# Kernel optimization log

Hardware: AMD Instinct MI355X
Metric: run time of the kernel (lower is better)

## Reference

```python
import jax, jax.numpy as jnp
import numpy as np

B, N, E = 16, 512, 6144          # graphs, sites/graph, edges/graph
D = 256                          # embed_dimension
RBF_DIM = 128
M = 6                            # num_messages
MAXZ = 84                        # max_atomic_num
INIT_MAX_DIST, INIT_GAP = 7.0, 30.0


def setup_inputs() -> dict:
    key = jax.random.key(0)
    ks = jax.random.split(key, 20)
    s = 0.02
    inp = {
        "site_class": jax.random.randint(ks[0], (B, N), 0, MAXZ, dtype=jnp.int64),
        "distance": jax.random.uniform(ks[1], (B, E), dtype=jnp.float32) * INIT_MAX_DIST,
        "connectivity": jax.random.randint(ks[2], (B, E, 2), 0, N, dtype=jnp.int64),
        # learned parameters
        "atom_emb": jax.random.normal(ks[3], (MAXZ, D), jnp.float32) * s,
        "mean_emb": jnp.zeros((MAXZ, 1), jnp.float32),  # Constant(output_bias=0.0)
        "centers": jnp.arange(RBF_DIM, dtype=jnp.float32) * (INIT_MAX_DIST / RBF_DIM),
        "gap": jnp.float32(INIT_GAP),
        "bond_W": jax.random.normal(ks[4], (RBF_DIM, D), jnp.float32) * s,
        "bond_b": jnp.zeros((D,), jnp.float32),
        "offset_W": jax.random.normal(ks[5], (D, 1), jnp.float32) * 1e-6,
        "offset_b": jnp.zeros((1,), jnp.float32),
        # per-message EdgeUpdate ConcatDense: Dense(2D, relu) -> Dense(D), input 3D
        "edge_W1": jax.random.normal(ks[6], (M, 3 * D, 2 * D), jnp.float32) * s,
        "edge_b1": jnp.zeros((M, 2 * D), jnp.float32),
        "edge_W2": jax.random.normal(ks[7], (M, 2 * D, D), jnp.float32) * s,
        "edge_b2": jnp.zeros((M, D), jnp.float32),
        # per-message NodeUpdate ConcatDense: input 2D
        "node_W1": jax.random.normal(ks[8], (M, 2 * D, 2 * D), jnp.float32) * s,
        "node_b1": jnp.zeros((M, 2 * D), jnp.float32),
        "node_W2": jax.random.normal(ks[9], (M, 2 * D, D), jnp.float32) * s,
        "node_b2": jnp.zeros((M, D), jnp.float32),
    }
    return inp


def _gather(x, idx):
    # x: [B, N, D], idx: [B, E] -> [B, E, D]
    return x[jnp.arange(x.shape[0])[:, None], idx]


def reference(site_class, distance, connectivity,
              atom_emb, mean_emb, centers, gap, bond_W, bond_b,
              offset_W, offset_b,
              edge_W1, edge_b1, edge_W2, edge_b2,
              node_W1, node_b1, node_W2, node_b2):
    atom_mask = site_class != 0                     # [B, N] (Embedding mask_zero)
    bond_mask = distance != 0.0                     # [B, E] (RBFExpansion mask)

    atom_state = atom_emb[site_class]               # [B, N, D]
    atom_mean = mean_emb[site_class]                # [B, N, 1]

    # RBF expansion: exp(-gap * (d - centers)^2), masked distances -> 1.0
    d = distance[..., None]
    d = jnp.where(d != 0.0, d, 1.0)
    rbf = jnp.exp(-((d - centers) ** 2) * gap)      # [B, E, RBF_DIM]
    bond_state = rbf @ bond_W + bond_b              # [B, E, D]

    bidx = jnp.arange(site_class.shape[0])[:, None]
    idx0 = connectivity[..., 0]                     # scatter target
    idx1 = connectivity[..., 1]                     # message source

    n_msg = edge_W1.shape[0]
    for i in range(n_msg):
        # EdgeUpdate: concat(bond, src_atom, tgt_atom) -> Dense(2D, relu) -> Dense(D)
        src = _gather(atom_state, idx1)
        tgt = _gather(atom_state, idx0)
        h = jnp.concatenate([bond_state, src, tgt], axis=-1)      # [B, E, 3D]
        h = jax.nn.relu(h @ edge_W1[i] + edge_b1[i])
        h = h @ edge_W2[i] + edge_b2[i]
        h = jnp.where(bond_mask[..., None], h, 0.0)
        bond_state = bond_state + h

        # NodeUpdate: concat(src_atom, bond) -> MLP -> segment-sum onto idx0
        src = _gather(atom_state, idx1)
        m = jnp.concatenate([src, bond_state], axis=-1)           # [B, E, 2D]
        m = jax.nn.relu(m @ node_W1[i] + node_b1[i])
        m = m @ node_W2[i] + node_b2[i]
        new_atom = jnp.zeros_like(atom_state).at[bidx, idx0].add(m)
        new_atom = jnp.where(atom_mask[..., None], new_atom, 0.0)
        atom_state = atom_state + new_atom

    atom_mean = atom_mean + (atom_state @ offset_W + offset_b)   # [B, N, 1]

    # masked global average pooling over sites
    mask_f = atom_mask[..., None].astype(atom_mean.dtype)
    pooled = jnp.sum(atom_mean * mask_f, axis=1) / jnp.sum(mask_f, axis=1)
    return pooled  # [B, 1]
```

## Files before the change

### kernel.cpp

```cpp
#include <hip/hip_runtime.h>
#include <hip/hip_bf16.h>
#include <stdint.h>
#include <stddef.h>

#define Bb 16
#define Nn 512
#define Ee 6144
#define Dd 256
#define ROWS (Bb * Ee)

typedef short bf16x8 __attribute__((ext_vector_type(8)));
typedef float f32x4 __attribute__((ext_vector_type(4)));

__device__ __forceinline__ unsigned short f2bf(float f) {
  union { float f; unsigned u; } v; v.f = f;
  return (unsigned short)((v.u + 0x7fffu + ((v.u >> 16) & 1u)) >> 16);
}
__device__ __forceinline__ float bf2f(unsigned short h) {
  union { unsigned u; float f; } v; v.u = ((unsigned)h) << 16;
  return v.f;
}

__device__ __forceinline__ void gload16(const void* g, void* l) {
  __builtin_amdgcn_global_load_lds(
      (const __attribute__((address_space(1))) void*)g,
      (__attribute__((address_space(3))) void*)l, 16, 0, 0);
}

__global__ void transpose_w(const float* __restrict__ in, unsigned short* __restrict__ out,
                            int K, int Ncol) {
  __shared__ float tile[32][33];
  const float* inb = in + (size_t)blockIdx.z * K * Ncol;
  unsigned short* outb = out + (size_t)blockIdx.z * K * Ncol;
  int bk = blockIdx.x * 32, bn = blockIdx.y * 32;
  int tx = threadIdx.x, ty = threadIdx.y;
#pragma unroll
  for (int i = 0; i < 32; i += 8)
    tile[ty + i][tx] = inb[(size_t)(bk + ty + i) * Ncol + (bn + tx)];
  __syncthreads();
#pragma unroll
  for (int i = 0; i < 32; i += 8)
    outb[(size_t)(bn + ty + i) * K + (bk + tx)] = f2bf(tile[tx][ty + i]);
}

__global__ void atom_init(const int* __restrict__ cls, const float* __restrict__ emb,
                          float* __restrict__ atom, unsigned short* __restrict__ atomBf) {
  int s_ = blockIdx.x, d = threadIdx.x;
  size_t o = (size_t)s_ * Dd + d;
  float v = emb[(size_t)cls[s_] * Dd + d];
  atom[o] = v;
  atomBf[o] = f2bf(v);
}

__global__ void atom_fix(const int* __restrict__ cls, const float* __restrict__ emb,
                         float* __restrict__ atom, unsigned short* __restrict__ atomBf) {
  int s_ = blockIdx.x, d = threadIdx.x;
  size_t o = (size_t)s_ * Dd + d;
  float v = (cls[s_] == 0) ? emb[d] : atom[o];
  atom[o] = v;
  atomBf[o] = f2bf(v);
}

__global__ __launch_bounds__(256, 2) void gemm_rbf(
    const unsigned short* __restrict__ Wt, const float* __restrict__ bias,
    const float* __restrict__ dist, const float* __restrict__ centers,
    const float* __restrict__ gapP, unsigned short* __restrict__ bondHi,
    unsigned short* __restrict__ bondLo) {
  __shared__ __align__(16) unsigned short lA[128 * 64];
  __shared__ __align__(16) unsigned short lB[128 * 64];
  const int t = threadIdx.x;
  const int bm = blockIdx.x * 128, bn = blockIdx.y * 128;
  const int srow = t & 127, skc = (t >> 7) * 32;
  const int m = bm + srow;
  float dval = dist[m]; if (dval == 0.f) dval = 1.f;
  float gapv = *gapP;
  const unsigned short* pBt = Wt + (size_t)(bn + srow) * 128 + skc;
  const int wid = t >> 6, lane = t & 63;
  const int wm = (wid & 1) * 64, wn = (wid >> 1) * 64;
  const int fr = lane & 15, fk0 = (lane >> 4) * 8;
  f32x4 acc[4][4] = {};
  for (int k0 = 0; k0 < 128; k0 += 64) {
    union __align__(16) { unsigned short us[32]; bf16x8 v[4]; } ab, bb;
#pragma unroll
    for (int j = 0; j < 32; j++) {
      float x = dval - centers[k0 + skc + j];
      ab.us[j] = f2bf(__expf(-gapv * x * x));
    }
    const bf16x8* s = (const bf16x8*)(pBt + k0);
#pragma unroll
    for (int c = 0; c < 4; c++) bb.v[c] = s[c];
    __syncthreads();
#pragma unroll
    for (int c = 0; c < 4; c++) {
      int byteo = (skc + c * 8) * 2;
      int swz = byteo ^ ((srow & 7) << 4);
      *(bf16x8*)((char*)lA + srow * 128 + swz) = ab.v[c];
      *(bf16x8*)((char*)lB + srow * 128 + swz) = bb.v[c];
    }
    __syncthreads();
#pragma unroll
    for (int kk = 0; kk < 64; kk += 32) {
      bf16x8 af[4], bfq[4];
#pragma unroll
      for (int f = 0; f < 4; f++) {
        int r = wm + f * 16 + fr;
        af[f] = *(const bf16x8*)((const char*)lA + r * 128 + (((kk + fk0) * 2) ^ ((r & 7) << 4)));
        int cq = wn + f * 16 + fr;
        bfq[f] = *(const bf16x8*)((const char*)lB + cq * 128 + (((kk + fk0) * 2) ^ ((cq & 7) << 4)));
      }
#pragma unroll
      for (int i = 0; i < 4; i++)
#pragma unroll
        for (int j = 0; j < 4; j++)
          acc[i][j] = __builtin_amdgcn_mfma_f32_16x16x32_bf16(af[i], bfq[j], acc[i][j], 0, 0, 0);
    }
  }
#pragma unroll
  for (int i = 0; i < 4; i++)
#pragma unroll
    for (int j = 0; j < 4; j++) {
      int gcol = bn + wn + j * 16 + fr;
      float bvv = bias[gcol];
#pragma unroll
      for (int v = 0; v < 4; v++) {
        int grow = bm + wm + i * 16 + (lane >> 4) * 4 + v;
        float val = acc[i][j][v] + bvv;
        size_t o = (size_t)grow * Dd + gcol;
        unsigned short hi = f2bf(val);
        bondHi[o] = hi;
        bondLo[o] = f2bf(val - bf2f(hi));
      }
    }
}

struct GP {
  const unsigned short* Wt;
  const float* bias;
  const unsigned short* bondHi;
  unsigned short* bondLo;
  const unsigned short* atomBf;
  const unsigned short* h1;
  const int* conn;
  const float* dist;
  unsigned short* outH1;
  unsigned short* outBondHi;
  float* atomMaster;
};

#define A_EDGE1 0
#define A_NODE1 1
#define A_H1    2
#define EP_H1RELU 0
#define EP_EDGE2  1
#define EP_NODE2  2

template <int K, int NC, int AL, int EP>
__global__ __launch_bounds__(512, 8) void gemm128(GP p) {
  __shared__ __align__(16) char lds[32768];
  constexpr int BOFF = 16384;
  const int t = threadIdx.x;
  const int w = t >> 6, l = t & 63;
  constexpr int NT = NC / 128;

  const int nwg = gridDim.x;
  const int q8 = nwg >> 3;
  const int sb = (blockIdx.x & 7) * q8 + (blockIdx.x >> 3);
  const int bn = (sb % NT) * 128;
  const int bm = (sb / NT) * 128;

  const int srow = t >> 2;
  const int schk = t & 3;
  const int sswz = (schk ^ ((srow >> 1) & 3)) << 4;

  const char* pA0; const char* pA1; const char* pA2;
  if (AL == A_H1) {
    pA0 = (const char*)p.h1 + (size_t)(bm + srow) * (K * 2) + sswz;
    pA1 = pA0; pA2 = pA0;
  } else {
    int gr = bm + srow;
    int b = gr / Ee;
    int i0 = p.conn[2 * gr], i1 = p.conn[2 * gr + 1];
    const char* bondRow = (const char*)p.bondHi + (size_t)gr * 512 + sswz;
    const char* srcRow  = (const char*)p.atomBf + ((size_t)b * Nn + i1) * 512 + sswz;
    const char* tgtRow  = (const char*)p.atomBf + ((size_t)b * Nn + i0) * 512 + sswz;
    if (AL == A_EDGE1) { pA0 = bondRow; pA1 = srcRow; pA2 = tgtRow; }
    else               { pA0 = srcRow;  pA1 = bondRow; pA2 = bondRow; }
  }
  const char* pB = (const char*)p.Wt + (size_t)(bn + srow) * (K * 2) + sswz;

  const int fr = l & 15;
  const int q4 = l >> 4;
  const int wm = (w >> 2) * 64;
  const int wn = (w & 3) * 32;

  f32x4 acc[4][2] = {};

  auto stage = [&](int pb, int k0) {
    const char* src;
    if (AL == A_H1)         src = pA0 + k0 * 2;
    else if (AL == A_EDGE1) { int s = k0 >> 8; src = (s == 0 ? pA0 : (s == 1 ? pA1 : pA2)) + (k0 & 255) * 2; }
    else                    src = (k0 < 256 ? pA0 : pA1) + (k0 & 255) * 2;
    gload16(src, lds + pb * 8192 + w * 1024);
    gload16(pB + k0 * 2, lds + BOFF + pb * 8192 + w * 1024);
  };

  auto compute = [&](int pb) {
    bf16x8 av[4], bv[2];
#pragma unroll
    for (int f = 0; f < 4; f++) {
      int r = wm + f * 16 + fr;
      av[f] = *(const bf16x8*)(lds + pb * 8192 + r * 64 + ((q4 ^ ((r >> 1) & 3)) << 4));
    }
#pragma unroll
    for (int n = 0; n < 2; n++) {
      int rq = wn + n * 16 + fr;
      bv[n] = *(const bf16x8*)(lds + BOFF + pb * 8192 + rq * 64 + ((q4 ^ ((rq >> 1) & 3)) << 4));
    }
#pragma unroll
    for (int f = 0; f < 4; f++)
#pragma unroll
      for (int n = 0; n < 2; n++)
        acc[f][n] = __builtin_amdgcn_mfma_f32_16x16x32_bf16(av[f], bv[n], acc[f][n], 0, 0, 0);
  };

  constexpr int nT = K / 32;
  stage(0, 0);
  __syncthreads();
  for (int tt = 0; tt < nT; tt++) {
    int pb = tt & 1;
    if (tt + 1 < nT) stage(pb ^ 1, (tt + 1) * 32);
    compute(pb);
    __syncthreads();
  }

  float bias2[2];
#pragma unroll
  for (int n = 0; n < 2; n++) bias2[n] = p.bias[bn + wn + n * 16 + fr];

#pragma unroll
  for (int f = 0; f < 4; f++) {
#pragma unroll
    for (int v = 0; v < 4; v++) {
      int grow = bm + wm + f * 16 + q4 * 4 + v;
      if (EP == EP_H1RELU) {
#pragma unroll
        for (int n = 0; n < 2; n++) {
          int gcol = bn + wn + n * 16 + fr;
          float val = acc[f][n][v] + bias2[n];
          p.outH1[(size_t)grow * 512 + gcol] = f2bf(fmaxf(val, 0.f));
        }
      } else if (EP == EP_EDGE2) {
        if (p.dist[grow] != 0.f) {
#pragma unroll
          for (int n = 0; n < 2; n++) {
            int gcol = bn + wn + n * 16 + fr;
            size_t o = (size_t)grow * Dd + gcol;
            float cur = bf2f(p.bondHi[o]) + bf2f(p.bondLo[o]);
            float nv = cur + acc[f][n][v] + bias2[n];
            unsigned short hi = f2bf(nv);
            p.outBondHi[o] = hi;
            p.bondLo[o] = f2bf(nv - bf2f(hi));
          }
        }
      } else {
        int b = grow / Ee;
        int tg = p.conn[2 * grow];
        float* dst = p.atomMaster + ((size_t)b * Nn + tg) * Dd;
#pragma unroll
        for (int n = 0; n < 2; n++) {
          int gcol = bn + wn + n * 16 + fr;
          atomicAdd(dst + gcol, acc[f][n][v] + bias2[n]);
        }
      }
    }
  }
}

__global__ void pool_k(const float* __restrict__ atom, const int* __restrict__ cls,
                       const float* __restrict__ meanEmb, const float* __restrict__ oW,
                       const float* __restrict__ ob, float* __restrict__ out) {
  __shared__ float w[Dd];
  __shared__ float red[256];
  __shared__ float redc[256];
  int b = blockIdx.x, t = threadIdx.x;
  w[t] = oW[t];
  __syncthreads();
  float sum = 0.f, cnt = 0.f;
  for (int n = t; n < Nn; n += 256) {
    int site = b * Nn + n;
    int c = cls[site];
    const float* a = atom + (size_t)site * Dd;
    float dot = 0.f;
    for (int d = 0; d < Dd; d++) dot += a[d] * w[d];
    if (c != 0) { sum += meanEmb[c] + dot + ob[0]; cnt += 1.f; }
  }
  red[t] = sum; redc[t] = cnt;
  __syncthreads();
  for (int s = 128; s > 0; s >>= 1) {
    if (t < s) { red[t] += red[t + s]; redc[t] += redc[t + s]; }
    __syncthreads();
  }
  if (t == 0) out[b] = red[0] / redc[0];
}

extern "C" void kernel_launch(void* const* d_in, const int* in_sizes, int n_in,
                              void* d_out, int out_size, void* d_ws, size_t ws_size,
                              hipStream_t stream) {
  const int* site_class = (const int*)d_in[0];
  const float* distance = (const float*)d_in[1];
  const int* conn       = (const int*)d_in[2];
  const float* atom_emb = (const float*)d_in[3];
  const float* mean_emb = (const float*)d_in[4];
  const float* centers  = (const float*)d_in[5];
  const float* gapP     = (const float*)d_in[6];
  const float* bond_W   = (const float*)d_in[7];
  const float* bond_b   = (const float*)d_in[8];
  const float* offset_W = (const float*)d_in[9];
  const float* offset_b = (const float*)d_in[10];
  const float* edge_W1  = (const float*)d_in[11];
  const float* edge_b1  = (const float*)d_in[12];
  const float* edge_W2  = (const float*)d_in[13];
  const float* edge_b2  = (const float*)d_in[14];
  const float* node_W1  = (const float*)d_in[15];
  const float* node_b1  = (const float*)d_in[16];
  const float* node_W2  = (const float*)d_in[17];
  const float* node_b2  = (const float*)d_in[18];

  char* ws = (char*)d_ws;
  float* atom            = (float*)(ws + 0);
  unsigned short* atomBf = (unsigned short*)(ws + 8388608);
  unsigned short* bondHi = (unsigned short*)(ws + 12582912);
  unsigned short* bondLo = (unsigned short*)(ws + 62914560);
  unsigned short* h1     = (unsigned short*)(ws + 113246208);
  unsigned short* bWT    = (unsigned short*)(ws + 213909504);
  unsigned short* eW1T   = (unsigned short*)(ws + 213975040);
  unsigned short* eW2T   = (unsigned short*)(ws + 218693632);
  unsigned short* nW1T   = (unsigned short*)(ws + 220266496);
  unsigned short* nW2T   = (unsigned short*)(ws + 223412224);

  dim3 tb(32, 8);
  transpose_w<<<dim3(4, 8, 1), tb, 0, stream>>>(bond_W, bWT, 128, 256);
  transpose_w<<<dim3(24, 16, 6), tb, 0, stream>>>(edge_W1, eW1T, 768, 512);
  transpose_w<<<dim3(16, 8, 6), tb, 0, stream>>>(edge_W2, eW2T, 512, 256);
  transpose_w<<<dim3(16, 16, 6), tb, 0, stream>>>(node_W1, nW1T, 512, 512);
  transpose_w<<<dim3(16, 8, 6), tb, 0, stream>>>(node_W2, nW2T, 512, 256);

  atom_init<<<Bb * Nn, 256, 0, stream>>>(site_class, atom_emb, atom, atomBf);
  gemm_rbf<<<dim3(768, 2), 256, 0, stream>>>(bWT, bond_b, distance, centers, gapP, bondHi, bondLo);

  GP base{};
  base.conn = conn; base.dist = distance;
  base.bondHi = bondHi; base.bondLo = bondLo; base.atomBf = atomBf; base.h1 = h1;
  base.outH1 = h1; base.outBondHi = bondHi; base.atomMaster = atom;

  for (int i = 0; i < 6; i++) {
    {
      GP q = base;
      q.Wt = eW1T + (size_t)i * 512 * 768; q.bias = edge_b1 + i * 512;
      gemm128<768, 512, A_EDGE1, EP_H1RELU><<<3072, 512, 0, stream>>>(q);
    }
    {
      GP q = base;
      q.Wt = eW2T + (size_t)i * 256 * 512; q.bias = edge_b2 + i * 256;
      gemm128<512, 256, A_H1, EP_EDGE2><<<1536, 512, 0, stream>>>(q);
    }
    {
      GP q = base;
      q.Wt = nW1T + (size_t)i * 512 * 512; q.bias = node_b1 + i * 512;
      gemm128<512, 512, A_NODE1, EP_H1RELU><<<3072, 512, 0, stream>>>(q);
    }
    {
      GP q = base;
      q.Wt = nW2T + (size_t)i * 256 * 512; q.bias = node_b2 + i * 256;
      gemm128<512, 256, A_H1, EP_NODE2><<<1536, 512, 0, stream>>>(q);
    }
    atom_fix<<<Bb * Nn, 256, 0, stream>>>(site_class, atom_emb, atom, atomBf);
  }

  pool_k<<<Bb, 256, 0, stream>>>(atom, site_class, mean_emb, offset_W, offset_b, (float*)d_out);
}
```

Measured before the change: 2.054 ms.

## Deepen GEMM LDS pipeline to four stages with explicit vmcnt waits

Replaces the double-buffered LDS loop with a four-slot ring that keeps three tiles of global-to-LDS loads in flight, using explicit s_waitcnt vmcnt counts and one barrier per iteration instead of full __syncthreads. It also raises wave priority around the MFMA block. The aim is to hide global load latency better. The cost is double the LDS (64KB) and a lowered launch-bounds occupancy hint, and the hand-counted vmcnt waits must match the loads issued in flight.

Result: no change. 2.016 ms (-1.9%).

```diff
diff --git a/kernel.cpp b/kernel.cpp
--- a/kernel.cpp
+++ b/kernel.cpp
@@ -155,9 +155,9 @@
 #define EP_NODE2  2
 
 template <int K, int NC, int AL, int EP>
-__global__ __launch_bounds__(512, 8) void gemm128(GP p) {
-  __shared__ __align__(16) char lds[32768];
-  constexpr int BOFF = 16384;
+__global__ __launch_bounds__(512, 4) void gemm128(GP p) {
+  __shared__ __align__(16) char lds[65536];
+  constexpr int BOFF = 32768;
   const int t = threadIdx.x;
   const int w = t >> 6, l = t & 63;
   constexpr int NT = NC / 128;
@@ -195,43 +195,54 @@
 
   f32x4 acc[4][2] = {};
 
-  auto stage = [&](int pb, int k0) {
+  auto stage = [&](int sl, int k0) {
     const char* src;
     if (AL == A_H1)         src = pA0 + k0 * 2;
     else if (AL == A_EDGE1) { int s = k0 >> 8; src = (s == 0 ? pA0 : (s == 1 ? pA1 : pA2)) + (k0 & 255) * 2; }
     else                    src = (k0 < 256 ? pA0 : pA1) + (k0 & 255) * 2;
-    gload16(src, lds + pb * 8192 + w * 1024);
-    gload16(pB + k0 * 2, lds + BOFF + pb * 8192 + w * 1024);
+    gload16(src, lds + sl * 8192 + w * 1024);
+    gload16(pB + k0 * 2, lds + BOFF + sl * 8192 + w * 1024);
   };
 
-  auto compute = [&](int pb) {
+  auto compute = [&](int sl) {
     bf16x8 av[4], bv[2];
 #pragma unroll
     for (int f = 0; f < 4; f++) {
       int r = wm + f * 16 + fr;
-      av[f] = *(const bf16x8*)(lds + pb * 8192 + r * 64 + ((q4 ^ ((r >> 1) & 3)) << 4));
+      av[f] = *(const bf16x8*)(lds + sl * 8192 + r * 64 + ((q4 ^ ((r >> 1) & 3)) << 4));
     }
 #pragma unroll
     for (int n = 0; n < 2; n++) {
       int rq = wn + n * 16 + fr;
-      bv[n] = *(const bf16x8*)(lds + BOFF + pb * 8192 + rq * 64 + ((q4 ^ ((rq >> 1) & 3)) << 4));
-    }
+      bv[n] = *(const bf16x8*)(lds + BOFF + sl * 8192 + rq * 64 + ((q4 ^ ((rq >> 1) & 3)) << 4));
+    }
+    __builtin_amdgcn_s_setprio(1);
 #pragma unroll
     for (int f = 0; f < 4; f++)
 #pragma unroll
       for (int n = 0; n < 2; n++)
         acc[f][n] = __builtin_amdgcn_mfma_f32_16x16x32_bf16(av[f], bv[n], acc[f][n], 0, 0, 0);
+    __builtin_amdgcn_s_setprio(0);
   };
 
   constexpr int nT = K / 32;
-  stage(0, 0);
-  __syncthreads();
-  for (int tt = 0; tt < nT; tt++) {
-    int pb = tt & 1;
-    if (tt + 1 < nT) stage(pb ^ 1, (tt + 1) * 32);
-    compute(pb);
-    __syncthreads();
-  }
+  stage(0, 0); stage(1, 32); stage(2, 64);
+
+  for (int tt = 0; tt < nT - 2; ++tt) {
+    asm volatile("s_waitcnt vmcnt(4)" ::: "memory");
+    __builtin_amdgcn_s_barrier();
+    __builtin_amdgcn_sched_barrier(0);
+    if (tt + 3 < nT) stage((tt + 3) & 3, (tt + 3) * 32);
+    compute(tt & 3);
+  }
+  asm volatile("s_waitcnt vmcnt(2)" ::: "memory");
+  __builtin_amdgcn_s_barrier();
+  __builtin_amdgcn_sched_barrier(0);
+  compute((nT - 2) & 3);
+  asm volatile("s_waitcnt vmcnt(0)" ::: "memory");
+  __builtin_amdgcn_s_barrier();
+  __builtin_amdgcn_sched_barrier(0);
+  compute((nT - 1) & 3);
 
   float bias2[2];
 #pragma unroll
```
